# Kernel tuning notes

Hardware: AMD Instinct MI355X
Metric: run time of the kernel (lower is better)

## Reference

```python
import jax, jax.numpy as jnp
import numpy as np

M, N, H, C = 50000, 50000, 32, 128
K, GROUPS = 15, 8
CPG = C // GROUPS           # 16, channels per group
RADIUS, SIGMA, INF = 2.5, 1.0, 1.0e6
EPS = 1e-5                  # GroupNorm eps
NEG_SLOPE = 0.1             # LeakyReLU slope in alpha MLP


def setup_inputs() -> dict:
    key = jax.random.key(0)
    ks = jax.random.split(key, 12)
    q_pts = jax.random.normal(ks[0], (M, 3), jnp.float32) * 5.0
    s_pts = q_pts  # same-resolution layer: q == s
    s_feats = jax.random.normal(ks[1], (N, C), jnp.float32)
    neighb_inds = jax.random.randint(ks[2], (M, H), 0, N + 1)  # N = padding index
    # kernel points: center + 14 points in a sphere of given radius
    kp = jax.random.normal(ks[3], (K, 3), jnp.float32)
    kp = kp / (jnp.linalg.norm(kp, axis=1, keepdims=True) + 1e-9) * RADIUS * 0.66
    k_pts = kp.at[0].set(0.0)
    # alpha MLP: Linear(C->C) + LeakyReLU + Linear(C->K*CPG)
    W1 = jax.random.normal(ks[4], (C, C), jnp.float32) * np.sqrt(2.0 / C)
    b1 = jnp.zeros((C,), jnp.float32)
    W2 = jax.random.normal(ks[5], (C, K * CPG), jnp.float32) * np.sqrt(2.0 / C)
    b2 = jnp.zeros((K * CPG,), jnp.float32)
    gn_w = jnp.ones((K * CPG,), jnp.float32)
    gn_b = jnp.zeros((K * CPG,), jnp.float32)
    return {"q_pts": q_pts, "s_pts": s_pts, "s_feats": s_feats,
            "neighb_inds": neighb_inds, "k_pts": k_pts,
            "W1": W1, "b1": b1, "W2": W2, "b2": b2,
            "gn_w": gn_w, "gn_b": gn_b}


def reference(q_pts, s_pts, s_feats, k_pts, W1, b1, W2, b2, gn_w, gn_b, neighb_inds):
    m = q_pts.shape[0]
    # ---- neighbor geometry (no_grad in original) ----
    s_pts_pad = jnp.concatenate([s_pts, jnp.full((1, 3), INF, s_pts.dtype)], 0)
    neighbors = s_pts_pad[neighb_inds] - q_pts[:, None, :]          # (M,H,3)
    sq = jnp.sum((neighbors[:, :, None, :] - k_pts) ** 2, -1)       # (M,H,K)
    nn_sq = jnp.min(sq, -1)                                         # (M,H)
    nn_1nn = jnp.argmin(sq, -1)                                     # (M,H)
    infl = jnp.clip(1.0 - jnp.sqrt(nn_sq) / SIGMA, 0.0)             # linear influence
    # ---- neighbor features gather (padding row = zeros) ----
    feats_pad = jnp.concatenate([s_feats, jnp.zeros((1, C), s_feats.dtype)], 0)
    neighbor_feats = feats_pad[neighb_inds]                         # (M,H,C)
    # ---- dynamic weights from center features (q==s -> pooled = s_feats) ----
    pooled = s_feats
    h = pooled @ W1 + b1
    h = jnp.where(h >= 0, h, NEG_SLOPE * h)                         # LeakyReLU(0.1)
    cw = (h @ W2 + b2).reshape(m, K, CPG)                           # (M,K,CPG)
    # GroupNorm(K groups over K*CPG channels), stats over (points, CPG) per group
    mu = jnp.mean(cw, axis=(0, 2), keepdims=True)
    var = jnp.var(cw, axis=(0, 2), keepdims=True)
    cw = (cw - mu) * jax.lax.rsqrt(var + EPS)
    cw = cw * gn_w.reshape(1, K, CPG) + gn_b.reshape(1, K, CPG)
    # ---- gather weights at nearest kernel point, modulate by influence ----
    nw = jnp.take_along_axis(cw, nn_1nn[:, :, None], axis=1)        # (M,H,CPG)
    nw = nw * infl[:, :, None]                                      # weight_act = identity
    # ---- multiply and sum over neighbors ----
    nf = neighbor_feats.reshape(m, H, CPG, GROUPS)
    out = jnp.sum(nf * nw[:, :, :, None], axis=1)                   # (M,CPG,GROUPS)
    return out.reshape(m, C)
```

## Files before the change

### kernel.cpp

```cpp
#include <hip/hip_runtime.h>
#include <hip/hip_bf16.h>

#define Mpts 50000
#define Npts 50000
#define Hn 32
#define Cc 128
#define Kk 15
#define NCW 240

typedef __attribute__((ext_vector_type(8))) short short8;
typedef __attribute__((ext_vector_type(4))) float f32x4;
typedef __attribute__((ext_vector_type(2))) float f32x2;
typedef unsigned int u32;

__device__ inline ushort f2bf(float f) {
  __hip_bfloat16 h = __float2bfloat16(f);
  return *reinterpret_cast<ushort*>(&h);
}

__global__ __launch_bounds__(256) void k0_pre(
    const float* __restrict__ sfeat, const float* __restrict__ W1,
    const float* __restrict__ W2, ushort* __restrict__ sfb,
    ushort* __restrict__ W1t, ushort* __restrict__ W2t,
    float* __restrict__ stats)
{
  __shared__ ushort TT[240][66];
  const int t = threadIdx.x;
  const int b = blockIdx.x;
  if (b < 3125) {
    const size_t base = ((size_t)b * 256 + t) * 8;
    float4 f0 = *(const float4*)(sfeat + base);
    float4 f1 = *(const float4*)(sfeat + base + 4);
    union { short8 v; ushort u[8]; } pk;
    pk.u[0] = f2bf(f0.x); pk.u[1] = f2bf(f0.y); pk.u[2] = f2bf(f0.z); pk.u[3] = f2bf(f0.w);
    pk.u[4] = f2bf(f1.x); pk.u[5] = f2bf(f1.y); pk.u[6] = f2bf(f1.z); pk.u[7] = f2bf(f1.w);
    *(short8*)(sfb + base) = pk.v;
  } else if (b < 3127) {
    const int k0 = (b - 3125) * 64;
#pragma unroll
    for (int i = 0; i < 32; ++i) {
      int e = t + i * 256;
      int r = e >> 7, c = e & 127;
      TT[c][r] = f2bf(W1[(size_t)(k0 + r) * Cc + c]);
    }
    __syncthreads();
    int n = t >> 1, half = t & 1;
    union { short8 v[4]; ushort u[32]; } pk;
#pragma unroll
    for (int i = 0; i < 32; ++i) pk.u[i] = TT[n][half * 32 + i];
#pragma unroll
    for (int q = 0; q < 4; ++q)
      *(short8*)(W1t + (size_t)n * Cc + k0 + half * 32 + q * 8) = pk.v[q];
  } else if (b < 3129) {
    const int k0 = (b - 3127) * 64;
    for (int i = 0; i < 60; ++i) {
      int e = t + i * 256;
      int r = e / 240, c = e % 240;
      TT[c][r] = f2bf(W2[(size_t)(k0 + r) * NCW + c]);
    }
    __syncthreads();
    if (t < 240) {
      union { short8 v[8]; ushort u[64]; } pk;
#pragma unroll
      for (int i = 0; i < 64; ++i) pk.u[i] = TT[t][i];
#pragma unroll
      for (int q = 0; q < 8; ++q)
        *(short8*)(W2t + (size_t)t * Cc + k0 + q * 8) = pk.v[q];
    }
  } else {
    if (t < 16) {
      short8 z = short8{0,0,0,0,0,0,0,0};
      *(short8*)(sfb + (size_t)Npts * Cc + t * 8) = z;
    }
    if (t < 128) {
      float4 z4 = make_float4(0.f, 0.f, 0.f, 0.f);
      *(float4*)(stats + t * 4) = z4;
    }
  }
}

__global__ __launch_bounds__(256, 3) void k1_mlp(
    const ushort* __restrict__ sfb, const ushort* __restrict__ W1t,
    const float* __restrict__ b1, const ushort* __restrict__ W2t,
    const float* __restrict__ b2, ushort* __restrict__ cw,
    float* __restrict__ stats)
{
  __shared__ __align__(16) ushort shA[64 * 128];
  __shared__ __align__(16) ushort shW[128 * 128];
  __shared__ float red[2][15][4];

  const int t = threadIdx.x;
  const int r0 = blockIdx.x * 64;
  const int wid = t >> 6, lane = t & 63;
  const int l16 = lane & 15, lq = lane >> 4;

  uint4 av[4];
#pragma unroll
  for (int p = 0; p < 4; ++p) {
    int id = p * 256 + t;
    int r = id >> 4, c = id & 15;
    int g = r0 + r; if (g > Mpts) g = Mpts;
    av[p] = *(const uint4*)(sfb + (size_t)g * Cc + c * 8);
  }
  uint4 wv[8];
#pragma unroll
  for (int p = 0; p < 8; ++p) {
    int id = p * 256 + t;
    int r = id >> 4, c = id & 15;
    wv[p] = *(const uint4*)(W1t + r * Cc + c * 8);
  }
  asm volatile("" :: "v"(wv[0].x), "v"(wv[1].x), "v"(wv[2].x), "v"(wv[3].x),
                     "v"(wv[4].x), "v"(wv[5].x), "v"(wv[6].x), "v"(wv[7].x),
                     "v"(av[0].x), "v"(av[1].x), "v"(av[2].x), "v"(av[3].x));
#pragma unroll
  for (int p = 0; p < 8; ++p) {
    int id = p * 256 + t;
    int r = id >> 4, c = id & 15;
    *(uint4*)((char*)shW + ((r * 256 + c * 16) ^ ((r & 7) << 4))) = wv[p];
  }
#pragma unroll
  for (int p = 0; p < 4; ++p) {
    int id = p * 256 + t;
    int r = id >> 4, c = id & 15;
    *(uint4*)((char*)shA + ((r * 256 + c * 16) ^ ((r & 7) << 4))) = av[p];
  }
  __syncthreads();

  const int arow = wid * 16 + l16;
  const int axor = (arow & 7) << 4;

  f32x4 acc1[8];
#pragma unroll
  for (int nt = 0; nt < 8; ++nt) acc1[nt] = f32x4{0.f, 0.f, 0.f, 0.f};
#pragma unroll
  for (int kt = 0; kt < 4; ++kt) {
    const int koff2 = (kt * 32 + lq * 8) * 2;
    short8 a = *(const short8*)((const char*)shA + ((arow * 256 + koff2) ^ axor));
#pragma unroll
    for (int nt = 0; nt < 8; ++nt) {
      int wrow = nt * 16 + l16;
      short8 b = *(const short8*)((const char*)shW + ((wrow * 256 + koff2) ^ ((wrow & 7) << 4)));
      acc1[nt] = __builtin_amdgcn_mfma_f32_16x16x32_bf16(a, b, acc1[nt], 0, 0, 0);
    }
  }
#pragma unroll
  for (int nt = 0; nt < 8; ++nt) {
    int col = nt * 16 + l16;
    float bias = b1[col];
#pragma unroll
    for (int reg = 0; reg < 4; ++reg) {
      float h = acc1[nt][reg] + bias;
      h = h >= 0.f ? h : 0.1f * h;
      int row = wid * 16 + lq * 4 + reg;
      int byte = ((row * 256) + col * 2) ^ ((row & 7) << 4);
      *(ushort*)((char*)shA + byte) = f2bf(h);
    }
  }

  float s[15], ss[15];
#pragma unroll
  for (int j = 0; j < 15; ++j) { s[j] = 0.f; ss[j] = 0.f; }

#pragma unroll
  for (int pass = 0; pass < 2; ++pass) {
    __syncthreads();
    const int NCH = pass ? 7 : 8;
    uint4 wv2[8];
#pragma unroll
    for (int p = 0; p < NCH; ++p) {
      int id = p * 256 + t;
      int r = id >> 4, c = id & 15;
      wv2[p] = *(const uint4*)(W2t + (size_t)(pass * 128 + r) * Cc + c * 8);
    }
    if (pass == 0)
      asm volatile("" :: "v"(wv2[0].x), "v"(wv2[1].x), "v"(wv2[2].x), "v"(wv2[3].x),
                         "v"(wv2[4].x), "v"(wv2[5].x), "v"(wv2[6].x), "v"(wv2[7].x));
    else
      asm volatile("" :: "v"(wv2[0].x), "v"(wv2[1].x), "v"(wv2[2].x), "v"(wv2[3].x),
                         "v"(wv2[4].x), "v"(wv2[5].x), "v"(wv2[6].x));
#pragma unroll
    for (int p = 0; p < NCH; ++p) {
      int id = p * 256 + t;
      int r = id >> 4, c = id & 15;
      *(uint4*)((char*)shW + ((r * 256 + c * 16) ^ ((r & 7) << 4))) = wv2[p];
    }
    __syncthreads();

    const int J0 = pass * 8, NJ = pass ? 7 : 8;
    f32x4 acc2[8];
#pragma unroll
    for (int j = 0; j < 8; ++j) acc2[j] = f32x4{0.f, 0.f, 0.f, 0.f};
#pragma unroll
    for (int kt = 0; kt < 4; ++kt) {
      const int koff2 = (kt * 32 + lq * 8) * 2;
      short8 a = *(const short8*)((const char*)shA + ((arow * 256 + koff2) ^ axor));
      for (int j = 0; j < NJ; ++j) {
        int wrow = j * 16 + l16;
        short8 b = *(const short8*)((const char*)shW + ((wrow * 256 + koff2) ^ ((wrow & 7) << 4)));
        acc2[j] = __builtin_amdgcn_mfma_f32_16x16x32_bf16(a, b, acc2[j], 0, 0, 0);
      }
    }
    for (int j = 0; j < NJ; ++j) {
      int col = (J0 + j) * 16 + l16;
      float bias = b2[col];
#pragma unroll
      for (int reg = 0; reg < 4; ++reg) {
        int grow = r0 + wid * 16 + lq * 4 + reg;
        if (grow < Mpts) {
          float v = acc2[j][reg] + bias;
          cw[(size_t)grow * NCW + col] = f2bf(v);
          s[J0 + j] += v; ss[J0 + j] += v * v;
        }
      }
    }
  }

#pragma unroll
  for (int j = 0; j < 15; ++j) {
    for (int off = 32; off > 0; off >>= 1) {
      s[j]  += __shfl_xor(s[j],  off);
      ss[j] += __shfl_xor(ss[j], off);
    }
  }
  if (lane == 0) {
#pragma unroll
    for (int j = 0; j < 15; ++j) { red[0][j][wid] = s[j]; red[1][j][wid] = ss[j]; }
  }
  __syncthreads();
  float* st = stats + (blockIdx.x & 7) * 64;
  if (t < 15) {
    float S = red[0][t][0] + red[0][t][1] + red[0][t][2] + red[0][t][3];
    atomicAdd(&st[t], S);
  } else if (t >= 32 && t < 47) {
    int j = t - 32;
    float SS = red[1][j][0] + red[1][j][1] + red[1][j][2] + red[1][j][3];
    atomicAdd(&st[32 + j], SS);
  }
}

__global__ __launch_bounds__(256) void k2_geom(
    const float* __restrict__ q_pts, const float* __restrict__ s_pts,
    const int* __restrict__ nb, const float* __restrict__ kp,
    const float* __restrict__ gn_w, const float* __restrict__ gn_b,
    const float* __restrict__ stats, u32* __restrict__ geomP,
    float* __restrict__ AtabG, float* __restrict__ BtabG)
{
  __shared__ float kpt[3][15];
  __shared__ float mus[16], rss[16];
  const int t = threadIdx.x;
  if (t < 45) kpt[t % 3][t / 3] = kp[t];
  __syncthreads();

  const int gtid = blockIdx.x * 256 + t;
  const int m = gtid >> 5;
  int idx = nb[gtid]; if (idx > Npts) idx = Npts;
  float qx = q_pts[m * 3 + 0], qy = q_pts[m * 3 + 1], qz = q_pts[m * 3 + 2];
  float px, py, pz;
  if (idx < Npts) { px = s_pts[idx * 3 + 0]; py = s_pts[idx * 3 + 1]; pz = s_pts[idx * 3 + 2]; }
  else            { px = 1.0e6f; py = 1.0e6f; pz = 1.0e6f; }
  float nx = px - qx, ny = py - qy, nz = pz - qz;
  int ksel = 0; float best = 1e30f;
#pragma unroll
  for (int k = 0; k < Kk; ++k) {
    float dx = nx - kpt[0][k], dy = ny - kpt[1][k], dz = nz - kpt[2][k];
    float d = dx * dx + dy * dy + dz * dz;
    if (d < best) { best = d; ksel = k; }
  }
  float infl = 1.f - sqrtf(best);
  infl = infl > 0.f ? infl : 0.f;
  geomP[gtid] = (__float_as_uint(infl) & 0xFFFFFFF0u) | (u32)ksel;

  if (blockIdx.x == 0) {
    if (t < 15) {
      float S = 0.f, SS = 0.f;
#pragma unroll
      for (int r = 0; r < 8; ++r) { S += stats[r * 64 + t]; SS += stats[r * 64 + 32 + t]; }
      const float inv = 1.0f / (16.0f * (float)Mpts);
      float mu = S * inv;
      float var = SS * inv - mu * mu;
      mus[t] = mu;
      rss[t] = rsqrtf(var + 1e-5f);
    }
    __syncthreads();
    if (t < 240) {
      int g = t >> 4;
      float a = rss[g] * gn_w[t];
      AtabG[t] = a;
      BtabG[t] = gn_b[t] - mus[g] * a;
    }
  }
}

__global__ __launch_bounds__(256) void k3_out(
    const ushort* __restrict__ sfb, const int* __restrict__ nb,
    const u32* __restrict__ geomP, const float* __restrict__ AtabG,
    const float* __restrict__ BtabG, const ushort* __restrict__ cw,
    float* __restrict__ out)
{
  __shared__ float Atab[255], Btab[255];
  __shared__ float wtab[4][2][8][33];
  const int t = threadIdx.x;
  if (t < 240) {
    int k = t >> 4, c = t & 15;
    Atab[k * 17 + c] = AtabG[t];
    Btab[k * 17 + c] = BtabG[t];
  }
  __syncthreads();

  const int half = (blockIdx.x >= 6250) ? 1 : 0;
  const int pblk = blockIdx.x - half * 6250;
  const int wid = t >> 6, lane = t & 63;
  const int mbase = pblk * 8 + wid * 2;
  const int gtid = pblk * 256 + t;
  const int ch = lane & 7, hlane = (lane >> 3) & 3, p = lane >> 5;
  const int half8 = half * 8;

  u32 g = geomP[gtid];
  int idxv = nb[gtid]; if (idxv > Npts) idxv = Npts;

  const uint4* fb = (const uint4*)sfb;
  uint4 fv[8];
#pragma unroll
  for (int j = 0; j < 8; ++j) {
    int ih = __shfl(idxv, (p << 5) | (hlane + 4 * j));
    fv[j] = fb[ih * 16 + half8 + ch];
  }

  {
    int h = lane >> 1, c0 = (lane & 1) * 4;
#pragma unroll
    for (int q = 0; q < 2; ++q) {
      u32 gp = __shfl((int)g, (q << 5) | h);
      int kh = gp & 15;
      float wI = __uint_as_float(gp & 0xFFFFFFF0u);
      uint2 cwv = *(const uint2*)(cw + (size_t)(mbase + q) * NCW + kh * 16 + half8 + c0);
      const float* Ar = &Atab[kh * 17 + half8 + c0];
      const float* Br = &Btab[kh * 17 + half8 + c0];
      float v0 = __uint_as_float(cwv.x << 16);
      float v1 = __uint_as_float(cwv.x & 0xffff0000u);
      float v2 = __uint_as_float(cwv.y << 16);
      float v3 = __uint_as_float(cwv.y & 0xffff0000u);
      wtab[wid][q][c0 + 0][h] = fmaf(v0, Ar[0], Br[0]) * wI;
      wtab[wid][q][c0 + 1][h] = fmaf(v1, Ar[1], Br[1]) * wI;
      wtab[wid][q][c0 + 2][h] = fmaf(v2, Ar[2], Br[2]) * wI;
      wtab[wid][q][c0 + 3][h] = fmaf(v3, Ar[3], Br[3]) * wI;
    }
  }

  asm volatile("" :: "v"(fv[0].x), "v"(fv[1].x), "v"(fv[2].x), "v"(fv[3].x),
                     "v"(fv[4].x), "v"(fv[5].x), "v"(fv[6].x), "v"(fv[7].x));

  f32x2 a0 = {0.f, 0.f}, a1 = {0.f, 0.f}, a2 = {0.f, 0.f}, a3 = {0.f, 0.f};
#pragma unroll
  for (int j = 0; j < 8; ++j) {
    float w = wtab[wid][p][ch][hlane + 4 * j];
    f32x2 w2 = {w, w};
    u32 ux = fv[j].x, uy = fv[j].y, uz = fv[j].z, uw = fv[j].w;
    f32x2 q0 = {__uint_as_float(ux << 16), __uint_as_float(ux & 0xffff0000u)};
    f32x2 q1 = {__uint_as_float(uy << 16), __uint_as_float(uy & 0xffff0000u)};
    f32x2 q2 = {__uint_as_float(uz << 16), __uint_as_float(uz & 0xffff0000u)};
    f32x2 q3 = {__uint_as_float(uw << 16), __uint_as_float(uw & 0xffff0000u)};
    a0 = __builtin_elementwise_fma(q0, w2, a0);
    a1 = __builtin_elementwise_fma(q1, w2, a1);
    a2 = __builtin_elementwise_fma(q2, w2, a2);
    a3 = __builtin_elementwise_fma(q3, w2, a3);
  }
#pragma unroll
  for (int off = 8; off <= 16; off <<= 1) {
    a0[0] += __shfl_xor(a0[0], off); a0[1] += __shfl_xor(a0[1], off);
    a1[0] += __shfl_xor(a1[0], off); a1[1] += __shfl_xor(a1[1], off);
    a2[0] += __shfl_xor(a2[0], off); a2[1] += __shfl_xor(a2[1], off);
    a3[0] += __shfl_xor(a3[0], off); a3[1] += __shfl_xor(a3[1], off);
  }
  if ((lane & 24) == 0) {
    float* op = out + (size_t)(mbase + p) * Cc + half * 64 + ch * 8;
    float4 o0; o0.x = a0[0]; o0.y = a0[1]; o0.z = a1[0]; o0.w = a1[1];
    float4 o1; o1.x = a2[0]; o1.y = a2[1]; o1.z = a3[0]; o1.w = a3[1];
    *(float4*)(op)     = o0;
    *(float4*)(op + 4) = o1;
  }
}

extern "C" void kernel_launch(void* const* d_in, const int* in_sizes, int n_in,
                              void* d_out, int out_size, void* d_ws, size_t ws_size,
                              hipStream_t stream) {
  const float* q_pts  = (const float*)d_in[0];
  const float* s_pts  = (const float*)d_in[1];
  const float* sfeat  = (const float*)d_in[2];
  const int*   nb     = (const int*)d_in[3];
  const float* kp     = (const float*)d_in[4];
  const float* W1     = (const float*)d_in[5];
  const float* b1     = (const float*)d_in[6];
  const float* W2     = (const float*)d_in[7];
  const float* b2     = (const float*)d_in[8];
  const float* gn_w   = (const float*)d_in[9];
  const float* gn_b   = (const float*)d_in[10];
  float* out   = (float*)d_out;

  char* wsb = (char*)d_ws;
  float*  stats = (float*)wsb;
  ushort* sfb   = (ushort*)(wsb + 4096);
  ushort* W1t   = (ushort*)(wsb + 12804352);
  ushort* W2t   = (ushort*)(wsb + 12837120);
  ushort* cwb   = (ushort*)(wsb + 12898560);
  u32*    geomP = (u32*)   (wsb + 36898560);
  float*  AtabG = (float*) (wsb + 43298560);
  float*  BtabG = (float*) (wsb + 43299520);

  k0_pre <<<3130, 256, 0, stream>>>(sfeat, W1, W2, sfb, W1t, W2t, stats);
  k1_mlp <<<(Mpts + 63) / 64, 256, 0, stream>>>(sfb, W1t, b1, W2t, b2, cwb, stats);
  k2_geom<<<6250, 256, 0, stream>>>(q_pts, s_pts, nb, kp, gn_w, gn_b, stats,
                                    geomP, AtabG, BtabG);
  k3_out <<<12500, 256, 0, stream>>>(sfb, nb, geomP, AtabG, BtabG, cwb, out);
}
```

Before: 114.4 us.

## Make MLP kernel persistent with resident W1/W2 in LDS and prefetched tiles

The MLP kernel becomes persistent: 256 blocks each load W1 and the full W2 into shared memory once, then loop over 64-row tiles with a stride of 256. The next tile's features are prefetched into registers while the current tile is computed, and the second GEMM runs in a single pass over all 15 column tiles. This removes the per-block reload of both weight matrices and one pass of barriers. In exchange, shared memory use grows to about 108KB and occupancy drops to one block per CU, with 15 accumulators held live.

```diff
diff --git a/kernel.cpp b/kernel.cpp
--- a/kernel.cpp
+++ b/kernel.cpp
@@ -7,6 +7,7 @@
 #define Cc 128
 #define Kk 15
 #define NCW 240
+#define NTILE 782
 
 typedef __attribute__((ext_vector_type(8))) short short8;
 typedef __attribute__((ext_vector_type(4))) float f32x4;
@@ -79,140 +80,162 @@
   }
 }
 
-__global__ __launch_bounds__(256, 3) void k1_mlp(
+__global__ __launch_bounds__(256, 1) void k1_mlp(
     const ushort* __restrict__ sfb, const ushort* __restrict__ W1t,
     const float* __restrict__ b1, const ushort* __restrict__ W2t,
     const float* __restrict__ b2, ushort* __restrict__ cw,
     float* __restrict__ stats)
 {
   __shared__ __align__(16) ushort shA[64 * 128];
-  __shared__ __align__(16) ushort shW[128 * 128];
+  __shared__ __align__(16) ushort shW1[128 * 128];
+  __shared__ __align__(16) ushort shW2[240 * 128];
   __shared__ float red[2][15][4];
 
   const int t = threadIdx.x;
-  const int r0 = blockIdx.x * 64;
   const int wid = t >> 6, lane = t & 63;
   const int l16 = lane & 15, lq = lane >> 4;
 
-  uint4 av[4];
-#pragma unroll
-  for (int p = 0; p < 4; ++p) {
-    int id = p * 256 + t;
-    int r = id >> 4, c = id & 15;
-    int g = r0 + r; if (g > Mpts) g = Mpts;
-    av[p] = *(const uint4*)(sfb + (size_t)g * Cc + c * 8);
-  }
-  uint4 wv[8];
-#pragma unroll
-  for (int p = 0; p < 8; ++p) {
-    int id = p * 256 + t;
-    int r = id >> 4, c = id & 15;
-    wv[p] = *(const uint4*)(W1t + r * Cc + c * 8);
-  }
-  asm volatile("" :: "v"(wv[0].x), "v"(wv[1].x), "v"(wv[2].x), "v"(wv[3].x),
-                     "v"(wv[4].x), "v"(wv[5].x), "v"(wv[6].x), "v"(wv[7].x),
-                     "v"(av[0].x), "v"(av[1].x), "v"(av[2].x), "v"(av[3].x));
-#pragma unroll
-  for (int p = 0; p < 8; ++p) {
-    int id = p * 256 + t;
-    int r = id >> 4, c = id & 15;
-    *(uint4*)((char*)shW + ((r * 256 + c * 16) ^ ((r & 7) << 4))) = wv[p];
-  }
-#pragma unroll
-  for (int p = 0; p < 4; ++p) {
-    int id = p * 256 + t;
-    int r = id >> 4, c = id & 15;
-    *(uint4*)((char*)shA + ((r * 256 + c * 16) ^ ((r & 7) << 4))) = av[p];
-  }
-  __syncthreads();
+  {
+    uint4 wv[8];
+#pragma unroll
+    for (int p = 0; p < 8; ++p) {
+      int id = p * 256 + t;
+      int r = id >> 4, c = id & 15;
+      wv[p] = *(const uint4*)(W1t + r * Cc + c * 8);
+    }
+    asm volatile("" :: "v"(wv[0].x), "v"(wv[1].x), "v"(wv[2].x), "v"(wv[3].x),
+                       "v"(wv[4].x), "v"(wv[5].x), "v"(wv[6].x), "v"(wv[7].x));
+#pragma unroll
+    for (int p = 0; p < 8; ++p) {
+      int id = p * 256 + t;
+      int r = id >> 4, c = id & 15;
+      *(uint4*)((char*)shW1 + ((r * 256 + c * 16) ^ ((r & 7) << 4))) = wv[p];
+    }
+#pragma unroll
+    for (int batch = 0; batch < 2; ++batch) {
+      const int NCH = batch ? 7 : 8;
+      uint4 w2[8];
+#pragma unroll
+      for (int p = 0; p < NCH; ++p) {
+        int id = (batch * 8 + p) * 256 + t;
+        int r = id >> 4, c = id & 15;
+        w2[p] = *(const uint4*)(W2t + r * Cc + c * 8);
+      }
+      if (batch == 0)
+        asm volatile("" :: "v"(w2[0].x), "v"(w2[1].x), "v"(w2[2].x), "v"(w2[3].x),
+                           "v"(w2[4].x), "v"(w2[5].x), "v"(w2[6].x), "v"(w2[7].x));
+      else
+        asm volatile("" :: "v"(w2[0].x), "v"(w2[1].x), "v"(w2[2].x), "v"(w2[3].x),
+                           "v"(w2[4].x), "v"(w2[5].x), "v"(w2[6].x));
+#pragma unroll
+      for (int p = 0; p < NCH; ++p) {
+        int id = (batch * 8 + p) * 256 + t;
+        int r = id >> 4, c = id & 15;
+        *(uint4*)((char*)shW2 + ((r * 256 + c * 16) ^ ((r & 7) << 4))) = w2[p];
+      }
+    }
+  }
 
   const int arow = wid * 16 + l16;
   const int axor = (arow & 7) << 4;
-
-  f32x4 acc1[8];
-#pragma unroll
-  for (int nt = 0; nt < 8; ++nt) acc1[nt] = f32x4{0.f, 0.f, 0.f, 0.f};
-#pragma unroll
-  for (int kt = 0; kt < 4; ++kt) {
-    const int koff2 = (kt * 32 + lq * 8) * 2;
-    short8 a = *(const short8*)((const char*)shA + ((arow * 256 + koff2) ^ axor));
-#pragma unroll
-    for (int nt = 0; nt < 8; ++nt) {
-      int wrow = nt * 16 + l16;
-      short8 b = *(const short8*)((const char*)shW + ((wrow * 256 + koff2) ^ ((wrow & 7) << 4)));
-      acc1[nt] = __builtin_amdgcn_mfma_f32_16x16x32_bf16(a, b, acc1[nt], 0, 0, 0);
-    }
-  }
-#pragma unroll
-  for (int nt = 0; nt < 8; ++nt) {
-    int col = nt * 16 + l16;
-    float bias = b1[col];
-#pragma unroll
-    for (int reg = 0; reg < 4; ++reg) {
-      float h = acc1[nt][reg] + bias;
-      h = h >= 0.f ? h : 0.1f * h;
-      int row = wid * 16 + lq * 4 + reg;
-      int byte = ((row * 256) + col * 2) ^ ((row & 7) << 4);
-      *(ushort*)((char*)shA + byte) = f2bf(h);
-    }
-  }
+  const int cid_r = ((t) >> 4), cid_c = t & 15;
+  float bias1[8], bias2[15];
+#pragma unroll
+  for (int nt = 0; nt < 8; ++nt) bias1[nt] = b1[nt * 16 + l16];
+#pragma unroll
+  for (int j = 0; j < 15; ++j)  bias2[j]  = b2[j * 16 + l16];
 
   float s[15], ss[15];
 #pragma unroll
   for (int j = 0; j < 15; ++j) { s[j] = 0.f; ss[j] = 0.f; }
 
-#pragma unroll
-  for (int pass = 0; pass < 2; ++pass) {
+  int tile = blockIdx.x;
+  uint4 av[4];
+#pragma unroll
+  for (int p = 0; p < 4; ++p) {
+    int r = cid_r + p * 16;
+    int g = tile * 64 + r; if (g > Mpts) g = Mpts;
+    av[p] = *(const uint4*)(sfb + (size_t)g * Cc + cid_c * 8);
+  }
+
+  while (tile < NTILE) {
+    const int r0 = tile * 64;
+    asm volatile("" :: "v"(av[0].x), "v"(av[1].x), "v"(av[2].x), "v"(av[3].x));
     __syncthreads();
-    const int NCH = pass ? 7 : 8;
-    uint4 wv2[8];
-#pragma unroll
-    for (int p = 0; p < NCH; ++p) {
-      int id = p * 256 + t;
-      int r = id >> 4, c = id & 15;
-      wv2[p] = *(const uint4*)(W2t + (size_t)(pass * 128 + r) * Cc + c * 8);
-    }
-    if (pass == 0)
-      asm volatile("" :: "v"(wv2[0].x), "v"(wv2[1].x), "v"(wv2[2].x), "v"(wv2[3].x),
-                         "v"(wv2[4].x), "v"(wv2[5].x), "v"(wv2[6].x), "v"(wv2[7].x));
-    else
-      asm volatile("" :: "v"(wv2[0].x), "v"(wv2[1].x), "v"(wv2[2].x), "v"(wv2[3].x),
-                         "v"(wv2[4].x), "v"(wv2[5].x), "v"(wv2[6].x));
-#pragma unroll
-    for (int p = 0; p < NCH; ++p) {
-      int id = p * 256 + t;
-      int r = id >> 4, c = id & 15;
-      *(uint4*)((char*)shW + ((r * 256 + c * 16) ^ ((r & 7) << 4))) = wv2[p];
+#pragma unroll
+    for (int p = 0; p < 4; ++p) {
+      int r = cid_r + p * 16;
+      *(uint4*)((char*)shA + ((r * 256 + cid_c * 16) ^ ((r & 7) << 4))) = av[p];
     }
     __syncthreads();
 
-    const int J0 = pass * 8, NJ = pass ? 7 : 8;
-    f32x4 acc2[8];
-#pragma unroll
-    for (int j = 0; j < 8; ++j) acc2[j] = f32x4{0.f, 0.f, 0.f, 0.f};
+    const int ntile = tile + 256;
+    uint4 nv[4];
+#pragma unroll
+    for (int p = 0; p < 4; ++p) {
+      int r = cid_r + p * 16;
+      int g = (ntile < NTILE) ? (ntile * 64 + r) : Mpts;
+      if (g > Mpts) g = Mpts;
+      nv[p] = *(const uint4*)(sfb + (size_t)g * Cc + cid_c * 8);
+    }
+
+    f32x4 acc1[8];
+#pragma unroll
+    for (int nt = 0; nt < 8; ++nt) acc1[nt] = f32x4{0.f, 0.f, 0.f, 0.f};
 #pragma unroll
     for (int kt = 0; kt < 4; ++kt) {
       const int koff2 = (kt * 32 + lq * 8) * 2;
       short8 a = *(const short8*)((const char*)shA + ((arow * 256 + koff2) ^ axor));
-      for (int j = 0; j < NJ; ++j) {
+#pragma unroll
+      for (int nt = 0; nt < 8; ++nt) {
+        int wrow = nt * 16 + l16;
+        short8 b = *(const short8*)((const char*)shW1 + ((wrow * 256 + koff2) ^ ((wrow & 7) << 4)));
+        acc1[nt] = __builtin_amdgcn_mfma_f32_16x16x32_bf16(a, b, acc1[nt], 0, 0, 0);
+      }
+    }
+#pragma unroll
+    for (int nt = 0; nt < 8; ++nt) {
+      int col = nt * 16 + l16;
+#pragma unroll
+      for (int reg = 0; reg < 4; ++reg) {
+        float h = acc1[nt][reg] + bias1[nt];
+        h = h >= 0.f ? h : 0.1f * h;
+        int row = wid * 16 + lq * 4 + reg;
+        int byte = ((row * 256) + col * 2) ^ ((row & 7) << 4);
+        *(ushort*)((char*)shA + byte) = f2bf(h);
+      }
+    }
+
+    f32x4 acc2[15];
+#pragma unroll
+    for (int j = 0; j < 15; ++j) acc2[j] = f32x4{0.f, 0.f, 0.f, 0.f};
+#pragma unroll
+    for (int kt = 0; kt < 4; ++kt) {
+      const int koff2 = (kt * 32 + lq * 8) * 2;
+      short8 a = *(const short8*)((const char*)shA + ((arow * 256 + koff2) ^ axor));
+#pragma unroll
+      for (int j = 0; j < 15; ++j) {
         int wrow = j * 16 + l16;
-        short8 b = *(const short8*)((const char*)shW + ((wrow * 256 + koff2) ^ ((wrow & 7) << 4)));
+        short8 b = *(const short8*)((const char*)shW2 + ((wrow * 256 + koff2) ^ ((wrow & 7) << 4)));
         acc2[j] = __builtin_amdgcn_mfma_f32_16x16x32_bf16(a, b, acc2[j], 0, 0, 0);
       }
     }
-    for (int j = 0; j < NJ; ++j) {
-      int col = (J0 + j) * 16 + l16;
-      float bias = b2[col];
+#pragma unroll
+    for (int j = 0; j < 15; ++j) {
+      int col = j * 16 + l16;
 #pragma unroll
       for (int reg = 0; reg < 4; ++reg) {
         int grow = r0 + wid * 16 + lq * 4 + reg;
         if (grow < Mpts) {
-          float v = acc2[j][reg] + bias;
+          float v = acc2[j][reg] + bias2[j];
           cw[(size_t)grow * NCW + col] = f2bf(v);
-          s[J0 + j] += v; ss[J0 + j] += v * v;
+          s[j] += v; ss[j] += v * v;
         }
       }
     }
+#pragma unroll
+    for (int p = 0; p < 4; ++p) av[p] = nv[p];
+    tile = ntile;
   }
 
 #pragma unroll
@@ -408,7 +431,7 @@
   float*  BtabG = (float*) (wsb + 43299520);
 
   k0_pre <<<3130, 256, 0, stream>>>(sfeat, W1, W2, sfb, W1t, W2t, stats);
-  k1_mlp <<<(Mpts + 63) / 64, 256, 0, stream>>>(sfb, W1t, b1, W2t, b2, cwb, stats);
+  k1_mlp <<<256, 256, 0, stream>>>(sfb, W1t, b1, W2t, b2, cwb, stats);
   k2_geom<<<6250, 256, 0, stream>>>(q_pts, s_pts, nb, kp, gn_w, gn_b, stats,
                                     geomP, AtabG, BtabG);
   k3_out <<<12500, 256, 0, stream>>>(sfb, nb, geomP, AtabG, BtabG, cwb, out);
```

Measured after the change: 132.8 us. 16.0% more time.

## Drop LDS staging in MLP kernel; load MFMA fragments directly and shuffle hidden layer

Applied to the files above, without the earlier changes.

The MLP kernel no longer stages the input features, W1 and W2 tiles in shared memory behind block barriers. Each wave loads its MFMA operand fragments straight from global memory, computes the first layer transposed so the hidden activations stay in registers, and rearranges them with cross-lane shuffles into the A-fragment layout for the second GEMM. All 15 output tiles are accumulated in registers in one pass. This removes the LDS traffic and syncthreads, at the cost of redundant per-wave global/L2 weight reads and more VGPRs (the occupancy hint of 3 is also dropped).

```diff
diff --git a/kernel.cpp b/kernel.cpp
--- a/kernel.cpp
+++ b/kernel.cpp
@@ -79,142 +79,117 @@
   }
 }
 
-__global__ __launch_bounds__(256, 3) void k1_mlp(
+__global__ __launch_bounds__(256) void k1_mlp(
     const ushort* __restrict__ sfb, const ushort* __restrict__ W1t,
     const float* __restrict__ b1, const ushort* __restrict__ W2t,
     const float* __restrict__ b2, ushort* __restrict__ cw,
     float* __restrict__ stats)
 {
-  __shared__ __align__(16) ushort shA[64 * 128];
-  __shared__ __align__(16) ushort shW[128 * 128];
   __shared__ float red[2][15][4];
-
   const int t = threadIdx.x;
-  const int r0 = blockIdx.x * 64;
   const int wid = t >> 6, lane = t & 63;
   const int l16 = lane & 15, lq = lane >> 4;
-
-  uint4 av[4];
-#pragma unroll
-  for (int p = 0; p < 4; ++p) {
-    int id = p * 256 + t;
-    int r = id >> 4, c = id & 15;
-    int g = r0 + r; if (g > Mpts) g = Mpts;
-    av[p] = *(const uint4*)(sfb + (size_t)g * Cc + c * 8);
-  }
-  uint4 wv[8];
-#pragma unroll
-  for (int p = 0; p < 8; ++p) {
-    int id = p * 256 + t;
-    int r = id >> 4, c = id & 15;
-    wv[p] = *(const uint4*)(W1t + r * Cc + c * 8);
-  }
-  asm volatile("" :: "v"(wv[0].x), "v"(wv[1].x), "v"(wv[2].x), "v"(wv[3].x),
-                     "v"(wv[4].x), "v"(wv[5].x), "v"(wv[6].x), "v"(wv[7].x),
-                     "v"(av[0].x), "v"(av[1].x), "v"(av[2].x), "v"(av[3].x));
-#pragma unroll
-  for (int p = 0; p < 8; ++p) {
-    int id = p * 256 + t;
-    int r = id >> 4, c = id & 15;
-    *(uint4*)((char*)shW + ((r * 256 + c * 16) ^ ((r & 7) << 4))) = wv[p];
-  }
-#pragma unroll
-  for (int p = 0; p < 4; ++p) {
-    int id = p * 256 + t;
-    int r = id >> 4, c = id & 15;
-    *(uint4*)((char*)shA + ((r * 256 + c * 16) ^ ((r & 7) << 4))) = av[p];
-  }
-  __syncthreads();
-
-  const int arow = wid * 16 + l16;
-  const int axor = (arow & 7) << 4;
+  const int r0w = blockIdx.x * 64 + wid * 16;
+
+  int gpt = r0w + l16; if (gpt > Mpts) gpt = Mpts;
+  const ushort* prow = sfb + (size_t)gpt * Cc;
+
+  uint4 bfr[4];
+#pragma unroll
+  for (int kt = 0; kt < 4; ++kt)
+    bfr[kt] = *(const uint4*)(prow + kt * 32 + lq * 8);
+  asm volatile("" :: "v"(bfr[0].x), "v"(bfr[1].x), "v"(bfr[2].x), "v"(bfr[3].x));
 
   f32x4 acc1[8];
 #pragma unroll
   for (int nt = 0; nt < 8; ++nt) acc1[nt] = f32x4{0.f, 0.f, 0.f, 0.f};
 #pragma unroll
   for (int kt = 0; kt < 4; ++kt) {
-    const int koff2 = (kt * 32 + lq * 8) * 2;
-    short8 a = *(const short8*)((const char*)shA + ((arow * 256 + koff2) ^ axor));
-#pragma unroll
-    for (int nt = 0; nt < 8; ++nt) {
-      int wrow = nt * 16 + l16;
-      short8 b = *(const short8*)((const char*)shW + ((wrow * 256 + koff2) ^ ((wrow & 7) << 4)));
-      acc1[nt] = __builtin_amdgcn_mfma_f32_16x16x32_bf16(a, b, acc1[nt], 0, 0, 0);
-    }
-  }
+    uint4 wf[8];
+#pragma unroll
+    for (int nt = 0; nt < 8; ++nt)
+      wf[nt] = *(const uint4*)(W1t + (size_t)(nt * 16 + l16) * Cc + kt * 32 + lq * 8);
+    asm volatile("" :: "v"(wf[0].x), "v"(wf[1].x), "v"(wf[2].x), "v"(wf[3].x),
+                       "v"(wf[4].x), "v"(wf[5].x), "v"(wf[6].x), "v"(wf[7].x));
+    short8 bb = *(short8*)&bfr[kt];
+#pragma unroll
+    for (int nt = 0; nt < 8; ++nt)
+      acc1[nt] = __builtin_amdgcn_mfma_f32_16x16x32_bf16(*(short8*)&wf[nt], bb, acc1[nt], 0, 0, 0);
+  }
+
+  u32 P[8][2];
 #pragma unroll
   for (int nt = 0; nt < 8; ++nt) {
-    int col = nt * 16 + l16;
-    float bias = b1[col];
+    float4 bv = *(const float4*)(b1 + nt * 16 + lq * 4);
+    float h0 = acc1[nt][0] + bv.x; h0 = h0 >= 0.f ? h0 : 0.1f * h0;
+    float h1 = acc1[nt][1] + bv.y; h1 = h1 >= 0.f ? h1 : 0.1f * h1;
+    float h2 = acc1[nt][2] + bv.z; h2 = h2 >= 0.f ? h2 : 0.1f * h2;
+    float h3 = acc1[nt][3] + bv.w; h3 = h3 >= 0.f ? h3 : 0.1f * h3;
+    P[nt][0] = (u32)f2bf(h0) | ((u32)f2bf(h1) << 16);
+    P[nt][1] = (u32)f2bf(h2) | ((u32)f2bf(h3) << 16);
+  }
+
+  const int srcE = ((lq & 1) << 5) + l16;
+  const int srcO = srcE + 16;
+  f32x4 acc2[15];
+#pragma unroll
+  for (int j = 0; j < 15; ++j) acc2[j] = f32x4{0.f, 0.f, 0.f, 0.f};
+
+#pragma unroll
+  for (int kt = 0; kt < 4; ++kt) {
+    uint4 w2a[8];
+#pragma unroll
+    for (int j = 0; j < 8; ++j)
+      w2a[j] = *(const uint4*)(W2t + (size_t)(j * 16 + l16) * Cc + kt * 32 + lq * 8);
+    asm volatile("" :: "v"(w2a[0].x), "v"(w2a[1].x), "v"(w2a[2].x), "v"(w2a[3].x),
+                       "v"(w2a[4].x), "v"(w2a[5].x), "v"(w2a[6].x), "v"(w2a[7].x));
+
+    u32 hf[4];
+#pragma unroll
+    for (int half = 0; half < 2; ++half) {
+      u32 pa = P[2 * kt][half], pb = P[2 * kt + 1][half];
+      u32 eA = (u32)__shfl((int)pa, srcE);
+      u32 eB = (u32)__shfl((int)pb, srcE);
+      u32 oA = (u32)__shfl((int)pa, srcO);
+      u32 oB = (u32)__shfl((int)pb, srcO);
+      hf[half]     = (lq & 2) ? eB : eA;
+      hf[2 + half] = (lq & 2) ? oB : oA;
+    }
+    uint4 hv; hv.x = hf[0]; hv.y = hf[1]; hv.z = hf[2]; hv.w = hf[3];
+    short8 hfrag = *(short8*)&hv;
+
+#pragma unroll
+    for (int j = 0; j < 8; ++j)
+      acc2[j] = __builtin_amdgcn_mfma_f32_16x16x32_bf16(hfrag, *(short8*)&w2a[j], acc2[j], 0, 0, 0);
+
+    uint4 w2b[7];
+#pragma unroll
+    for (int j = 0; j < 7; ++j)
+      w2b[j] = *(const uint4*)(W2t + (size_t)((8 + j) * 16 + l16) * Cc + kt * 32 + lq * 8);
+    asm volatile("" :: "v"(w2b[0].x), "v"(w2b[1].x), "v"(w2b[2].x), "v"(w2b[3].x),
+                       "v"(w2b[4].x), "v"(w2b[5].x), "v"(w2b[6].x));
+#pragma unroll
+    for (int j = 0; j < 7; ++j)
+      acc2[8 + j] = __builtin_amdgcn_mfma_f32_16x16x32_bf16(hfrag, *(short8*)&w2b[j], acc2[8 + j], 0, 0, 0);
+  }
+
+  float s[15], ss[15];
+#pragma unroll
+  for (int j = 0; j < 15; ++j) { s[j] = 0.f; ss[j] = 0.f; }
+#pragma unroll
+  for (int j = 0; j < 15; ++j) {
+    int col = j * 16 + l16;
+    float bias = b2[col];
 #pragma unroll
     for (int reg = 0; reg < 4; ++reg) {
-      float h = acc1[nt][reg] + bias;
-      h = h >= 0.f ? h : 0.1f * h;
-      int row = wid * 16 + lq * 4 + reg;
-      int byte = ((row * 256) + col * 2) ^ ((row & 7) << 4);
-      *(ushort*)((char*)shA + byte) = f2bf(h);
-    }
-  }
-
-  float s[15], ss[15];
-#pragma unroll
-  for (int j = 0; j < 15; ++j) { s[j] = 0.f; ss[j] = 0.f; }
-
-#pragma unroll
-  for (int pass = 0; pass < 2; ++pass) {
-    __syncthreads();
-    const int NCH = pass ? 7 : 8;
-    uint4 wv2[8];
-#pragma unroll
-    for (int p = 0; p < NCH; ++p) {
-      int id = p * 256 + t;
-      int r = id >> 4, c = id & 15;
-      wv2[p] = *(const uint4*)(W2t + (size_t)(pass * 128 + r) * Cc + c * 8);
-    }
-    if (pass == 0)
-      asm volatile("" :: "v"(wv2[0].x), "v"(wv2[1].x), "v"(wv2[2].x), "v"(wv2[3].x),
-                         "v"(wv2[4].x), "v"(wv2[5].x), "v"(wv2[6].x), "v"(wv2[7].x));
-    else
-      asm volatile("" :: "v"(wv2[0].x), "v"(wv2[1].x), "v"(wv2[2].x), "v"(wv2[3].x),
-                         "v"(wv2[4].x), "v"(wv2[5].x), "v"(wv2[6].x));
-#pragma unroll
-    for (int p = 0; p < NCH; ++p) {
-      int id = p * 256 + t;
-      int r = id >> 4, c = id & 15;
-      *(uint4*)((char*)shW + ((r * 256 + c * 16) ^ ((r & 7) << 4))) = wv2[p];
-    }
-    __syncthreads();
-
-    const int J0 = pass * 8, NJ = pass ? 7 : 8;
-    f32x4 acc2[8];
-#pragma unroll
-    for (int j = 0; j < 8; ++j) acc2[j] = f32x4{0.f, 0.f, 0.f, 0.f};
-#pragma unroll
-    for (int kt = 0; kt < 4; ++kt) {
-      const int koff2 = (kt * 32 + lq * 8) * 2;
-      short8 a = *(const short8*)((const char*)shA + ((arow * 256 + koff2) ^ axor));
-      for (int j = 0; j < NJ; ++j) {
-        int wrow = j * 16 + l16;
-        short8 b = *(const short8*)((const char*)shW + ((wrow * 256 + koff2) ^ ((wrow & 7) << 4)));
-        acc2[j] = __builtin_amdgcn_mfma_f32_16x16x32_bf16(a, b, acc2[j], 0, 0, 0);
+      int grow = r0w + lq * 4 + reg;
+      if (grow < Mpts) {
+        float v = acc2[j][reg] + bias;
+        cw[(size_t)grow * NCW + col] = f2bf(v);
+        s[j] += v; ss[j] += v * v;
       }
     }
-    for (int j = 0; j < NJ; ++j) {
-      int col = (J0 + j) * 16 + l16;
-      float bias = b2[col];
-#pragma unroll
-      for (int reg = 0; reg < 4; ++reg) {
-        int grow = r0 + wid * 16 + lq * 4 + reg;
-        if (grow < Mpts) {
-          float v = acc2[j][reg] + bias;
-          cw[(size_t)grow * NCW + col] = f2bf(v);
-          s[J0 + j] += v; ss[J0 + j] += v * v;
-        }
-      }
-    }
-  }
-
+  }
 #pragma unroll
   for (int j = 0; j < 15; ++j) {
     for (int off = 32; off > 0; off >>= 1) {
```

After: 139.7 us. +22.1%, slower.
